# Optimization experiments

Measured on AMD Instinct MI355X. Metric: run time of the kernel, lower is better.

## Reference

```python
import jax, jax.numpy as jnp
import numpy as np

B, N, T, F_IN = 4, 2000, 24, 16
H = 128          # hidden_dim
E = 64000        # num edges
C = 6            # num_classes (LOS A-F)
NH = 1           # num_horizons


def setup_inputs() -> dict:
    key = jax.random.key(0)
    ks = jax.random.split(key, 16)
    s = lambda *sh: 1.0 / np.sqrt(sh[-1])
    inp = {
        "node_features": jax.random.normal(ks[0], (B, N, T, F_IN), dtype=jnp.float32),
        "edge_index": jax.random.randint(ks[1], (2, E), 0, N, dtype=jnp.int64),
        # GRU (single layer, unidirectional), PyTorch gate order r,z,n
        "W_ih": jax.random.normal(ks[2], (3 * H, F_IN), dtype=jnp.float32) * s(3 * H, F_IN),
        "W_hh": jax.random.normal(ks[3], (3 * H, H), dtype=jnp.float32) * s(3 * H, H),
        "b_ih": jnp.zeros((3 * H,), dtype=jnp.float32),
        "b_hh": jnp.zeros((3 * H,), dtype=jnp.float32),
        # two GCN layers (H -> H)
        "gcn_W1": jax.random.normal(ks[4], (H, H), dtype=jnp.float32) * s(H, H),
        "gcn_b1": jnp.zeros((H,), dtype=jnp.float32),
        "gcn_W2": jax.random.normal(ks[5], (H, H), dtype=jnp.float32) * s(H, H),
        "gcn_b2": jnp.zeros((H,), dtype=jnp.float32),
        # LayerNorms
        "ln_g1": jnp.ones((H,), dtype=jnp.float32),
        "ln_b1": jnp.zeros((H,), dtype=jnp.float32),
        "ln_g2": jnp.ones((H,), dtype=jnp.float32),
        "ln_b2": jnp.zeros((H,), dtype=jnp.float32),
        # classifier: Linear(2H -> H), ReLU, Linear(H -> C*NH)
        "cls_W1": jax.random.normal(ks[6], (H, 2 * H), dtype=jnp.float32) * s(H, 2 * H),
        "cls_b1": jnp.zeros((H,), dtype=jnp.float32),
        "cls_W2": jax.random.normal(ks[7], (C * NH, H), dtype=jnp.float32) * s(C * NH, H),
        "cls_b2": jnp.zeros((C * NH,), dtype=jnp.float32),
    }
    return inp


def _gru(x, W_ih, W_hh, b_ih, b_hh):
    # x: [BN, T, F] -> final hidden [BN, H]
    BN = x.shape[0]
    gi = jnp.einsum('btf,gf->btg', x, W_ih) + b_ih           # [BN, T, 3H]
    h0 = jnp.zeros((BN, H), dtype=x.dtype)

    def step(h, gi_t):
        gh = h @ W_hh.T + b_hh
        ir, iz, inn = jnp.split(gi_t, 3, axis=-1)
        hr, hz, hn = jnp.split(gh, 3, axis=-1)
        r = jax.nn.sigmoid(ir + hr)
        z = jax.nn.sigmoid(iz + hz)
        n = jnp.tanh(inn + r * hn)
        h_new = (1.0 - z) * n + z * h
        return h_new, None

    h_fin, _ = jax.lax.scan(step, h0, jnp.swapaxes(gi, 0, 1))  # scan over time
    return h_fin


def _gcn(x, src, dst, W, b):
    # x: [B, N, D]; normalized adjacency aggregation then linear
    deg = jax.ops.segment_sum(jnp.ones((src.shape[0],), x.dtype), dst, num_segments=N)
    deg = jnp.maximum(deg, 1.0)
    dis = deg ** -0.5
    norm = dis[src] * dis[dst]                                # [E]
    msg = x[:, src, :] * norm[None, :, None]                  # [B, E, D]
    agg = jax.vmap(lambda m: jax.ops.segment_sum(m, dst, num_segments=N))(msg)
    return agg @ W.T + b


def _layernorm(x, g, b, eps=1e-5):
    mu = jnp.mean(x, axis=-1, keepdims=True)
    var = jnp.var(x, axis=-1, keepdims=True)
    return (x - mu) * jax.lax.rsqrt(var + eps) * g + b


def reference(node_features, edge_index, W_ih, W_hh, b_ih, b_hh,
              gcn_W1, gcn_b1, gcn_W2, gcn_b2,
              ln_g1, ln_b1, ln_g2, ln_b2,
              cls_W1, cls_b1, cls_W2, cls_b2):
    src, dst = edge_index[0], edge_index[1]
    x = node_features.reshape(B * N, T, F_IN)
    temporal = _gru(x, W_ih, W_hh, b_ih, b_hh).reshape(B, N, H)   # [B, N, H]

    s = _gcn(temporal, src, dst, gcn_W1, gcn_b1)
    s = jax.nn.relu(_layernorm(s, ln_g1, ln_b1))
    s = _gcn(s, src, dst, gcn_W2, gcn_b2)
    s = jax.nn.relu(_layernorm(s, ln_g2, ln_b2))

    combined = jnp.concatenate([temporal, s], axis=-1)            # [B, N, 2H]
    h = jax.nn.relu(combined @ cls_W1.T + cls_b1)
    logits = h @ cls_W2.T + cls_b2
    return logits.reshape(B, N, NH, C)
```

## Files before the change

### kernel.cpp

```cpp
#include <hip/hip_runtime.h>
#include <math.h>

#define BB  4
#define NN  2000
#define TT  24
#define FIN 16
#define HH  128
#define EE  64000
#define CC  6
#define BN  (BB*NN)

typedef _Float16 f16x8 __attribute__((ext_vector_type(8)));
typedef float f32x4 __attribute__((ext_vector_type(4)));

__global__ __launch_bounds__(256) void prep_kernel(
    const int* __restrict__ dst, int* __restrict__ cnt,
    const float* __restrict__ gW2, const float* __restrict__ cW1,
    float* __restrict__ o2, _Float16* __restrict__ o3)
{
    const int b = blockIdx.x;
    const int tid = threadIdx.x;
    if (b < 250) {
        int e = b * 256 + tid;
        atomicAdd(&cnt[dst[e]], 1);
    } else if (b < 314) {
        int idx = (b - 250) * 256 + tid;
        int r = idx >> 7, c = idx & 127;
        o2[c * 128 + r] = gW2[idx];
    } else {
        int idx = (b - 314) * 256 + tid;
        int r = idx >> 8, c = idx & 255;
        o3[c * 128 + r] = (_Float16)cW1[idx];
    }
}

__global__ __launch_bounds__(256) void scan_kernel(
    const int* __restrict__ cnt,
    int* __restrict__ rowptr, int* __restrict__ cursor, float* __restrict__ dis)
{
    __shared__ int part[256];
    int tid = threadIdx.x;
    int base = tid * 8;
    int loc[8]; int s = 0;
    #pragma unroll
    for (int u = 0; u < 8; ++u) {
        int v = (base + u < NN) ? cnt[base + u] : 0;
        loc[u] = s; s += v;
    }
    part[tid] = s;
    __syncthreads();
    #pragma unroll
    for (int off = 1; off < 256; off <<= 1) {
        int add = (tid >= off) ? part[tid - off] : 0;
        __syncthreads();
        part[tid] += add;
        __syncthreads();
    }
    int offset = (tid > 0) ? part[tid - 1] : 0;
    #pragma unroll
    for (int u = 0; u < 8; ++u) {
        int idx = base + u;
        if (idx < NN) {
            rowptr[idx] = offset + loc[u];
            cursor[idx] = offset + loc[u];
            dis[idx] = rsqrtf(fmaxf((float)cnt[idx], 1.0f));
        }
    }
    if (tid == 255) rowptr[NN] = part[255];
}

#define HP2 136
#define GRUB 500

__global__ __launch_bounds__(512) void gru_csr_kernel(
    const float* __restrict__ x,
    const float* __restrict__ W_hh,
    const float* __restrict__ W_ih,
    const float* __restrict__ b_ih, const float* __restrict__ b_hh,
    const float* __restrict__ gW1,
    _Float16* __restrict__ t16,
    _Float16* __restrict__ tw16,
    const int* __restrict__ src, const int* __restrict__ dst,
    const float* __restrict__ dis, int* __restrict__ cursor,
    int* __restrict__ esrc, float* __restrict__ enorm)
{
    const int tid  = threadIdx.x;

    if (blockIdx.x >= GRUB) {
        int e = (blockIdx.x - GRUB) * 512 + tid;
        if (e < EE) {
            int d = dst[e], s = src[e];
            int pos = atomicAdd(&cursor[d], 1);
            esrc[pos] = s;
            enorm[pos] = dis[s] * dis[d];
        }
        return;
    }

    const int lane = tid & 63;
    const int w    = tid >> 6;
    const int l15  = lane & 15;
    const int lg   = lane >> 4;
    const int m0   = blockIdx.x * 16;
    const int u    = w * 16 + l15;

    __shared__ __align__(16) unsigned short Hhi[2][16][HP2];
    __shared__ __align__(16) unsigned short Xhi[TT][16][FIN];

    f16x8 Bh[3][4];
    #pragma unroll
    for (int g = 0; g < 3; ++g) {
        const int col = g * 128 + u;
        #pragma unroll
        for (int kf = 0; kf < 4; ++kf) {
            const float* wp = W_hh + col * 128 + kf * 32 + lg * 8;
            float4 c0 = *(const float4*)wp;
            float4 c1 = *(const float4*)(wp + 4);
            f16x8 b;
            b[0] = (_Float16)c0.x; b[1] = (_Float16)c0.y;
            b[2] = (_Float16)c0.z; b[3] = (_Float16)c0.w;
            b[4] = (_Float16)c1.x; b[5] = (_Float16)c1.y;
            b[6] = (_Float16)c1.z; b[7] = (_Float16)c1.w;
            Bh[g][kf] = b;
        }
    }
    f16x8 Bi[3];
    #pragma unroll
    for (int g = 0; g < 3; ++g) {
        const int col = g * 128 + u;
        f16x8 b;
        #pragma unroll
        for (int i = 0; i < 8; ++i) b[i] = (_Float16)0.0f;
        if (lg < 2) {
            const float* wp = W_ih + col * 16 + lg * 8;
            float4 c0 = *(const float4*)wp;
            float4 c1 = *(const float4*)(wp + 4);
            b[0] = (_Float16)c0.x; b[1] = (_Float16)c0.y;
            b[2] = (_Float16)c0.z; b[3] = (_Float16)c0.w;
            b[4] = (_Float16)c1.x; b[5] = (_Float16)c1.y;
            b[6] = (_Float16)c1.z; b[7] = (_Float16)c1.w;
        } else if (lg == 2) {
            float bias = b_ih[col] + ((g < 2) ? b_hh[col] : 0.0f);
            b[0] = (_Float16)bias;
        }
        Bi[g] = b;
    }

    const float bhn = b_hh[256 + u];
    float hprev[4] = {0.0f, 0.0f, 0.0f, 0.0f};

    for (int i = tid; i < TT * 16 * FIN; i += 512) {
        int t   = i >> 8;
        int rem = i & 255;
        int seq = rem >> 4;
        int f   = rem & 15;
        float v = x[(size_t)(m0 + seq) * (TT * FIN) + t * FIN + f];
        _Float16 hb = (_Float16)v;
        Xhi[t][seq][f] = *(unsigned short*)&hb;
    }
    for (int i = tid; i < 16 * HP2; i += 512) (&Hhi[0][0][0])[i] = 0;
    __syncthreads();

    const f32x4 Z4 = (f32x4){0.f, 0.f, 0.f, 0.f};
    f32x4 aR, aZ, aH, aI;

#define IH_SHADOW(tt) do { \
        f16x8 axh; \
        _Float16 zz = (_Float16)0.0f; \
        axh = (f16x8){zz,zz,zz,zz,zz,zz,zz,zz}; \
        if (lg < 2) { \
            axh = *(const f16x8*)&Xhi[tt][l15][lg * 8]; \
        } else if (lg == 2) { \
            axh[0] = (_Float16)1.0f; \
        } \
        aR = __builtin_amdgcn_mfma_f32_16x16x32_f16(axh, Bi[0], Z4, 0, 0, 0); \
        aZ = __builtin_amdgcn_mfma_f32_16x16x32_f16(axh, Bi[1], Z4, 0, 0, 0); \
        aI = __builtin_amdgcn_mfma_f32_16x16x32_f16(axh, Bi[2], Z4, 0, 0, 0); \
        aH = Z4; \
    } while (0)

    IH_SHADOW(0);

    for (int t = 0; t < TT; ++t) {
        const int rb = t & 1, wb = rb ^ 1;

        #pragma unroll
        for (int kf = 0; kf < 4; ++kf) {
            const int ko = kf * 32 + lg * 8;
            f16x8 ahh = *(const f16x8*)&Hhi[rb][l15][ko];
            aR = __builtin_amdgcn_mfma_f32_16x16x32_f16(ahh, Bh[0][kf], aR, 0, 0, 0);
            aZ = __builtin_amdgcn_mfma_f32_16x16x32_f16(ahh, Bh[1][kf], aZ, 0, 0, 0);
            aH = __builtin_amdgcn_mfma_f32_16x16x32_f16(ahh, Bh[2][kf], aH, 0, 0, 0);
        }

        f32x4 aRv = aR, aZv = aZ, aHv = aH, aIv = aI;

        #pragma unroll
        for (int p = 0; p < 4; ++p) {
            float r = __builtin_amdgcn_rcpf(1.0f + __expf(-aRv[p]));
            float z = __builtin_amdgcn_rcpf(1.0f + __expf(-aZv[p]));
            float pre = fmaf(r, aHv[p] + bhn, aIv[p]);
            float e2 = __expf(2.0f * pre);
            float n = fmaf(-2.0f, __builtin_amdgcn_rcpf(e2 + 1.0f), 1.0f);
            float h = fmaf(z, hprev[p] - n, n);
            hprev[p] = h;
            _Float16 hb = (_Float16)h;
            const int seq = lg * 4 + p;
            Hhi[wb][seq][u] = *(unsigned short*)&hb;
        }

        if (t + 1 < TT) IH_SHADOW(t + 1);
        __syncthreads();
    }
#undef IH_SHADOW

    #pragma unroll
    for (int p = 0; p < 4; ++p)
        t16[(size_t)(m0 + lg * 4 + p) * HH + u] = (_Float16)hprev[p];

    {
        f32x4 acc = Z4;
        #pragma unroll
        for (int kf = 0; kf < 4; ++kf) {
            const float* wp = gW1 + (size_t)u * 128 + kf * 32 + lg * 8;
            float4 c0 = *(const float4*)wp;
            float4 c1 = *(const float4*)(wp + 4);
            f16x8 b;
            b[0] = (_Float16)c0.x; b[1] = (_Float16)c0.y;
            b[2] = (_Float16)c0.z; b[3] = (_Float16)c0.w;
            b[4] = (_Float16)c1.x; b[5] = (_Float16)c1.y;
            b[6] = (_Float16)c1.z; b[7] = (_Float16)c1.w;
            f16x8 ah = *(const f16x8*)&Hhi[0][l15][kf * 32 + lg * 8];
            acc = __builtin_amdgcn_mfma_f32_16x16x32_f16(ah, b, acc, 0, 0, 0);
        }
        #pragma unroll
        for (int p = 0; p < 4; ++p) {
            const int row = lg * 4 + p;
            tw16[(size_t)(m0 + row) * HH + u] = (_Float16)acc[p];
        }
    }
}

__global__ __launch_bounds__(256) void gcn1_kernel(
    const _Float16* __restrict__ xin,
    const int* __restrict__ rowptr,
    const int* __restrict__ esrc,
    const float* __restrict__ enorm,
    const float* __restrict__ bias,
    const float* __restrict__ gma, const float* __restrict__ bta,
    _Float16* __restrict__ out)
{
    const int n = blockIdx.x;
    const int tid = threadIdx.x;
    const int j = tid & 127;
    const int half = tid >> 7;
    const int beg = rowptr[n], end = rowptr[n + 1];
    const int len = end - beg;
    const int mid = beg + ((len + 1) >> 1);
    int e        = half ? mid : beg;
    const int e1 = half ? end : mid;

    float a0 = 0.f, a1 = 0.f, a2 = 0.f, a3 = 0.f;
    for (; e + 1 < e1; e += 2) {
        int   s0 = esrc[e],   s1 = esrc[e + 1];
        float m0 = enorm[e],  m1 = enorm[e + 1];
        const _Float16* p0 = xin + (size_t)s0 * HH + j;
        const _Float16* p1 = xin + (size_t)s1 * HH + j;
        a0 = fmaf(m0, (float)p0[0],       a0); a1 = fmaf(m0, (float)p0[NN*HH],   a1);
        a2 = fmaf(m0, (float)p0[2*NN*HH], a2); a3 = fmaf(m0, (float)p0[3*NN*HH], a3);
        a0 = fmaf(m1, (float)p1[0],       a0); a1 = fmaf(m1, (float)p1[NN*HH],   a1);
        a2 = fmaf(m1, (float)p1[2*NN*HH], a2); a3 = fmaf(m1, (float)p1[3*NN*HH], a3);
    }
    if (e < e1) {
        int s0 = esrc[e]; float m0 = enorm[e];
        const _Float16* p0 = xin + (size_t)s0 * HH + j;
        a0 = fmaf(m0, (float)p0[0],       a0); a1 = fmaf(m0, (float)p0[NN*HH],   a1);
        a2 = fmaf(m0, (float)p0[2*NN*HH], a2); a3 = fmaf(m0, (float)p0[3*NN*HH], a3);
    }

    __shared__ __align__(16) float agg[BB][HH];
    __shared__ __align__(16) float pagg[BB][HH];
    if (half) {
        pagg[0][j] = a0; pagg[1][j] = a1; pagg[2][j] = a2; pagg[3][j] = a3;
    }
    __syncthreads();
    if (!half) {
        agg[0][j] = a0 + pagg[0][j]; agg[1][j] = a1 + pagg[1][j];
        agg[2][j] = a2 + pagg[2][j]; agg[3][j] = a3 + pagg[3][j];
    }
    __syncthreads();

    const float bj = bias[j];
    const int b0 = half * 2, b1 = half * 2 + 1;
    float c0 = agg[b0][j] + bj;
    float c1 = agg[b1][j] + bj;

    const int lane = tid & 63, wv_ = (tid >> 6) & 1;
    __shared__ float red[2][2][2][2];
    {
        float s1 = c0, s2 = c0 * c0;
        for (int off = 32; off >= 1; off >>= 1) { s1 += __shfl_down(s1, off); s2 += __shfl_down(s2, off); }
        if (lane == 0) { red[half][wv_][0][0] = s1; red[half][wv_][0][1] = s2; }
        s1 = c1; s2 = c1 * c1;
        for (int off = 32; off >= 1; off >>= 1) { s1 += __shfl_down(s1, off); s2 += __shfl_down(s2, off); }
        if (lane == 0) { red[half][wv_][1][0] = s1; red[half][wv_][1][1] = s2; }
    }
    __syncthreads();

    const float gj = gma[j], btj = bta[j];
    #pragma unroll
    for (int q = 0; q < 2; ++q) {
        float cv = q ? c1 : c0;
        float s1 = red[half][0][q][0] + red[half][1][q][0];
        float s2 = red[half][0][q][1] + red[half][1][q][1];
        float mu = s1 * (1.0f / HH);
        float var = s2 * (1.0f / HH) - mu * mu;
        float y = (cv - mu) * rsqrtf(var + 1e-5f) * gj + btj;
        out[((size_t)(half * 2 + q) * NN + n) * HH + j] = (_Float16)fmaxf(y, 0.0f);
    }
}

__global__ __launch_bounds__(256) void gcn2_kernel(
    const _Float16* __restrict__ xin,
    const int* __restrict__ rowptr,
    const int* __restrict__ esrc,
    const float* __restrict__ enorm,
    const float* __restrict__ Wt,
    const float* __restrict__ bias,
    const float* __restrict__ gma, const float* __restrict__ bta,
    _Float16* __restrict__ out)
{
    const int n = blockIdx.x;
    const int tid = threadIdx.x;
    const int j = tid & 127;
    const int half = tid >> 7;
    const int beg = rowptr[n], end = rowptr[n + 1];
    const int len = end - beg;
    const int mid = beg + ((len + 1) >> 1);
    int e        = half ? mid : beg;
    const int e1 = half ? end : mid;

    float a0 = 0.f, a1 = 0.f, a2 = 0.f, a3 = 0.f;
    for (; e + 1 < e1; e += 2) {
        int   s0 = esrc[e],   s1 = esrc[e + 1];
        float m0 = enorm[e],  m1 = enorm[e + 1];
        const _Float16* p0 = xin + (size_t)s0 * HH + j;
        const _Float16* p1 = xin + (size_t)s1 * HH + j;
        a0 = fmaf(m0, (float)p0[0],       a0); a1 = fmaf(m0, (float)p0[NN*HH],   a1);
        a2 = fmaf(m0, (float)p0[2*NN*HH], a2); a3 = fmaf(m0, (float)p0[3*NN*HH], a3);
        a0 = fmaf(m1, (float)p1[0],       a0); a1 = fmaf(m1, (float)p1[NN*HH],   a1);
        a2 = fmaf(m1, (float)p1[2*NN*HH], a2); a3 = fmaf(m1, (float)p1[3*NN*HH], a3);
    }
    if (e < e1) {
        int s0 = esrc[e]; float m0 = enorm[e];
        const _Float16* p0 = xin + (size_t)s0 * HH + j;
        a0 = fmaf(m0, (float)p0[0],       a0); a1 = fmaf(m0, (float)p0[NN*HH],   a1);
        a2 = fmaf(m0, (float)p0[2*NN*HH], a2); a3 = fmaf(m0, (float)p0[3*NN*HH], a3);
    }

    __shared__ __align__(16) float agg[BB][HH];
    __shared__ __align__(16) float pagg[BB][HH];
    if (half) {
        pagg[0][j] = a0; pagg[1][j] = a1; pagg[2][j] = a2; pagg[3][j] = a3;
    }
    __syncthreads();
    if (!half) {
        agg[0][j] = a0 + pagg[0][j]; agg[1][j] = a1 + pagg[1][j];
        agg[2][j] = a2 + pagg[2][j]; agg[3][j] = a3 + pagg[3][j];
    }
    __syncthreads();

    const float bj = bias[j];
    const int b0 = half * 2, b1 = half * 2 + 1;
    float c0 = bj, c1 = bj;
    #pragma unroll 4
    for (int k = 0; k < HH; ++k) {
        float wv = Wt[k * HH + j];
        c0 = fmaf(wv, agg[b0][k], c0);
        c1 = fmaf(wv, agg[b1][k], c1);
    }

    const int lane = tid & 63, wv_ = (tid >> 6) & 1;
    __shared__ float red[2][2][2][2];
    {
        float s1 = c0, s2 = c0 * c0;
        for (int off = 32; off >= 1; off >>= 1) { s1 += __shfl_down(s1, off); s2 += __shfl_down(s2, off); }
        if (lane == 0) { red[half][wv_][0][0] = s1; red[half][wv_][0][1] = s2; }
        s1 = c1; s2 = c1 * c1;
        for (int off = 32; off >= 1; off >>= 1) { s1 += __shfl_down(s1, off); s2 += __shfl_down(s2, off); }
        if (lane == 0) { red[half][wv_][1][0] = s1; red[half][wv_][1][1] = s2; }
    }
    __syncthreads();

    const float gj = gma[j], btj = bta[j];
    #pragma unroll
    for (int q = 0; q < 2; ++q) {
        float cv = q ? c1 : c0;
        float s1 = red[half][0][q][0] + red[half][1][q][0];
        float s2 = red[half][0][q][1] + red[half][1][q][1];
        float mu = s1 * (1.0f / HH);
        float var = s2 * (1.0f / HH) - mu * mu;
        float y = (cv - mu) * rsqrtf(var + 1e-5f) * gj + btj;
        out[((size_t)(half * 2 + q) * NN + n) * HH + j] = (_Float16)fmaxf(y, 0.0f);
    }
}

__global__ __launch_bounds__(512) void cls_kernel(
    const _Float16* __restrict__ t16,
    const _Float16* __restrict__ s2,
    const _Float16* __restrict__ c16,
    const float* __restrict__ b1,
    const float* __restrict__ W2,
    const float* __restrict__ b2,
    float* __restrict__ out)
{
    const int tid  = threadIdx.x;
    const int lane = tid & 63;
    const int w    = tid >> 6;
    const int l15  = lane & 15;
    const int lg   = lane >> 4;
    const int r0   = blockIdx.x * 16;
    const int u    = w * 16 + l15;

    const f32x4 Z4 = (f32x4){0.f, 0.f, 0.f, 0.f};
    f32x4 acc = Z4;

    #pragma unroll
    for (int kf = 0; kf < 8; ++kf) {
        const int kl = (kf & 3) * 32 + lg * 8;
        const _Float16* ap = (kf < 4) ? (t16 + (size_t)(r0 + l15) * HH + kl)
                                      : (s2  + (size_t)(r0 + l15) * HH + kl);
        f16x8 a = *(const f16x8*)ap;
        f16x8 b;
        const int kg = kf * 32 + lg * 8;
        #pragma unroll
        for (int i = 0; i < 8; ++i) b[i] = c16[(size_t)(kg + i) * 128 + u];
        acc = __builtin_amdgcn_mfma_f32_16x16x32_f16(a, b, acc, 0, 0, 0);
    }

    __shared__ __align__(16) float h1L[16][HH];
    const float bu = b1[u];
    #pragma unroll
    for (int p = 0; p < 4; ++p) {
        const int row = lg * 4 + p;
        h1L[row][u] = fmaxf(acc[p] + bu, 0.0f);
    }
    __syncthreads();

    if (tid < 16 * CC) {
        int r = tid / CC, c = tid - r * CC;
        float a = b2[c];
        const float* wp = W2 + c * HH;
        #pragma unroll 4
        for (int k = 0; k < HH; ++k) a = fmaf(wp[k], h1L[r][k], a);
        out[(size_t)(r0 + r) * CC + c] = a;
    }
}

extern "C" void kernel_launch(void* const* d_in, const int* in_sizes, int n_in,
                              void* d_out, int out_size, void* d_ws, size_t ws_size,
                              hipStream_t stream) {
    const float* x    = (const float*)d_in[0];
    const int*   ei   = (const int*)  d_in[1];
    const float* W_ih = (const float*)d_in[2];
    const float* W_hh = (const float*)d_in[3];
    const float* b_ih = (const float*)d_in[4];
    const float* b_hh = (const float*)d_in[5];
    const float* gW1  = (const float*)d_in[6];
    const float* gb1  = (const float*)d_in[7];
    const float* gW2  = (const float*)d_in[8];
    const float* gb2  = (const float*)d_in[9];
    const float* lg1  = (const float*)d_in[10];
    const float* lb1  = (const float*)d_in[11];
    const float* lg2  = (const float*)d_in[12];
    const float* lb2  = (const float*)d_in[13];
    const float* cW1  = (const float*)d_in[14];
    const float* cb1  = (const float*)d_in[15];
    const float* cW2  = (const float*)d_in[16];
    const float* cb2  = (const float*)d_in[17];
    float* out = (float*)d_out;

    float* ws = (float*)d_ws;
    float* Wt_g2 = ws;  ws += 128 * 128;
    float* dis   = ws;  ws += 2048;
    float* enorm = ws;  ws += EE;
    _Float16* t16  = (_Float16*)ws;  ws += (size_t)BN * HH / 2;
    _Float16* tw16 = (_Float16*)ws;  ws += (size_t)BN * HH / 2;
    _Float16* s16  = (_Float16*)ws;  ws += (size_t)BN * HH / 2;
    _Float16* s2_16= (_Float16*)ws;  ws += (size_t)BN * HH / 2;
    _Float16* c16  = (_Float16*)ws;  ws += 256 * 128 / 2;
    int* ip      = (int*)ws;
    int* cnt     = ip;  ip += 2048;
    int* rowptr  = ip;  ip += 2080;
    int* cursor  = ip;  ip += 2048;
    int* esrc    = ip;  ip += EE;

    const int* srcp = ei;
    const int* dstp = ei + EE;

    hipMemsetAsync(cnt, 0, 2048 * sizeof(int), stream);

    prep_kernel<<<442, 256, 0, stream>>>(dstp, cnt, gW2, cW1, Wt_g2, c16);
    scan_kernel<<<1, 256, 0, stream>>>(cnt, rowptr, cursor, dis);

    gru_csr_kernel<<<GRUB + EE / 512, 512, 0, stream>>>(
        x, W_hh, W_ih, b_ih, b_hh, gW1, t16, tw16,
        srcp, dstp, dis, cursor, esrc, enorm);

    gcn1_kernel<<<NN, 256, 0, stream>>>(tw16, rowptr, esrc, enorm,
                                        gb1, lg1, lb1, s16);

    gcn2_kernel<<<NN, 256, 0, stream>>>(s16, rowptr, esrc, enorm,
                                        Wt_g2, gb2, lg2, lb2, s2_16);

    cls_kernel<<<BN / 16, 512, 0, stream>>>(t16, s2_16, c16, cb1, cW2, cb2, out);
}
```

Measured before the change: 115.0 us.

## Fuse GCN2 weight transform into GCN1 and classifier into GCN2 aggregation

The GCN2 weight matmul moves ahead of aggregation and onto MFMA at the end of the GCN1 kernel, so GCN2 aggregates pre-transformed features. The temporal half of the classifier's first linear layer is computed in the GRU epilogue, and the separate classifier kernel is folded into the GCN2 kernel. The prep-time weight transposes and the t16/s16 intermediates are dropped. This saves a launch, several intermediate buffers and a scalar FMA loop, at the cost of uncoalesced weight loads and fewer, larger blocks (4 nodes each, one 128-thread group per node, no edge splitting).

```diff
diff --git a/kernel.cpp b/kernel.cpp
--- a/kernel.cpp
+++ b/kernel.cpp
@@ -14,24 +14,10 @@
 typedef float f32x4 __attribute__((ext_vector_type(4)));
 
 __global__ __launch_bounds__(256) void prep_kernel(
-    const int* __restrict__ dst, int* __restrict__ cnt,
-    const float* __restrict__ gW2, const float* __restrict__ cW1,
-    float* __restrict__ o2, _Float16* __restrict__ o3)
+    const int* __restrict__ dst, int* __restrict__ cnt)
 {
-    const int b = blockIdx.x;
-    const int tid = threadIdx.x;
-    if (b < 250) {
-        int e = b * 256 + tid;
-        atomicAdd(&cnt[dst[e]], 1);
-    } else if (b < 314) {
-        int idx = (b - 250) * 256 + tid;
-        int r = idx >> 7, c = idx & 127;
-        o2[c * 128 + r] = gW2[idx];
-    } else {
-        int idx = (b - 314) * 256 + tid;
-        int r = idx >> 8, c = idx & 255;
-        o3[c * 128 + r] = (_Float16)cW1[idx];
-    }
+    int e = blockIdx.x * 256 + threadIdx.x;
+    atomicAdd(&cnt[dst[e]], 1);
 }
 
 __global__ __launch_bounds__(256) void scan_kernel(
@@ -78,8 +64,9 @@
     const float* __restrict__ W_ih,
     const float* __restrict__ b_ih, const float* __restrict__ b_hh,
     const float* __restrict__ gW1,
-    _Float16* __restrict__ t16,
+    const float* __restrict__ cW1,
     _Float16* __restrict__ tw16,
+    _Float16* __restrict__ tc16,
     const int* __restrict__ src, const int* __restrict__ dst,
     const float* __restrict__ dis, int* __restrict__ cursor,
     int* __restrict__ esrc, float* __restrict__ enorm)
@@ -214,58 +201,66 @@
     }
 #undef IH_SHADOW
 
-    #pragma unroll
-    for (int p = 0; p < 4; ++p)
-        t16[(size_t)(m0 + lg * 4 + p) * HH + u] = (_Float16)hprev[p];
-
     {
-        f32x4 acc = Z4;
+        f32x4 accw = Z4, accc = Z4;
         #pragma unroll
         for (int kf = 0; kf < 4; ++kf) {
-            const float* wp = gW1 + (size_t)u * 128 + kf * 32 + lg * 8;
+            const int ko = kf * 32 + lg * 8;
+            f16x8 ah = *(const f16x8*)&Hhi[0][l15][ko];
+
+            const float* wp = gW1 + (size_t)u * 128 + ko;
             float4 c0 = *(const float4*)wp;
             float4 c1 = *(const float4*)(wp + 4);
-            f16x8 b;
-            b[0] = (_Float16)c0.x; b[1] = (_Float16)c0.y;
-            b[2] = (_Float16)c0.z; b[3] = (_Float16)c0.w;
-            b[4] = (_Float16)c1.x; b[5] = (_Float16)c1.y;
-            b[6] = (_Float16)c1.z; b[7] = (_Float16)c1.w;
-            f16x8 ah = *(const f16x8*)&Hhi[0][l15][kf * 32 + lg * 8];
-            acc = __builtin_amdgcn_mfma_f32_16x16x32_f16(ah, b, acc, 0, 0, 0);
+            f16x8 bw;
+            bw[0] = (_Float16)c0.x; bw[1] = (_Float16)c0.y;
+            bw[2] = (_Float16)c0.z; bw[3] = (_Float16)c0.w;
+            bw[4] = (_Float16)c1.x; bw[5] = (_Float16)c1.y;
+            bw[6] = (_Float16)c1.z; bw[7] = (_Float16)c1.w;
+            accw = __builtin_amdgcn_mfma_f32_16x16x32_f16(ah, bw, accw, 0, 0, 0);
+
+            const float* cp = cW1 + (size_t)u * 256 + ko;
+            float4 d0 = *(const float4*)cp;
+            float4 d1 = *(const float4*)(cp + 4);
+            f16x8 bc;
+            bc[0] = (_Float16)d0.x; bc[1] = (_Float16)d0.y;
+            bc[2] = (_Float16)d0.z; bc[3] = (_Float16)d0.w;
+            bc[4] = (_Float16)d1.x; bc[5] = (_Float16)d1.y;
+            bc[6] = (_Float16)d1.z; bc[7] = (_Float16)d1.w;
+            accc = __builtin_amdgcn_mfma_f32_16x16x32_f16(ah, bc, accc, 0, 0, 0);
         }
         #pragma unroll
         for (int p = 0; p < 4; ++p) {
             const int row = lg * 4 + p;
-            tw16[(size_t)(m0 + row) * HH + u] = (_Float16)acc[p];
-        }
-    }
-}
-
-__global__ __launch_bounds__(256) void gcn1_kernel(
-    const _Float16* __restrict__ xin,
+            tw16[(size_t)(m0 + row) * HH + u] = (_Float16)accw[p];
+            tc16[(size_t)(m0 + row) * HH + u] = (_Float16)accc[p];
+        }
+    }
+}
+
+__global__ __launch_bounds__(512) void gcn1b_kernel(
+    const _Float16* __restrict__ tw,
     const int* __restrict__ rowptr,
     const int* __restrict__ esrc,
     const float* __restrict__ enorm,
-    const float* __restrict__ bias,
-    const float* __restrict__ gma, const float* __restrict__ bta,
-    _Float16* __restrict__ out)
+    const float* __restrict__ gb1,
+    const float* __restrict__ lg1, const float* __restrict__ lb1,
+    const float* __restrict__ gW2,
+    _Float16* __restrict__ sw)
 {
-    const int n = blockIdx.x;
     const int tid = threadIdx.x;
-    const int j = tid & 127;
-    const int half = tid >> 7;
-    const int beg = rowptr[n], end = rowptr[n + 1];
-    const int len = end - beg;
-    const int mid = beg + ((len + 1) >> 1);
-    int e        = half ? mid : beg;
-    const int e1 = half ? end : mid;
+    const int nd  = tid >> 7;
+    const int j   = tid & 127;
+    const int n0  = blockIdx.x * 4;
+    const int n   = n0 + nd;
 
     float a0 = 0.f, a1 = 0.f, a2 = 0.f, a3 = 0.f;
+    int e = rowptr[n];
+    const int e1 = rowptr[n + 1];
     for (; e + 1 < e1; e += 2) {
-        int   s0 = esrc[e],   s1 = esrc[e + 1];
-        float m0 = enorm[e],  m1 = enorm[e + 1];
-        const _Float16* p0 = xin + (size_t)s0 * HH + j;
-        const _Float16* p1 = xin + (size_t)s1 * HH + j;
+        int   s0 = esrc[e],   s1i = esrc[e + 1];
+        float m0 = enorm[e],  m1  = enorm[e + 1];
+        const _Float16* p0 = tw + (size_t)s0  * HH + j;
+        const _Float16* p1 = tw + (size_t)s1i * HH + j;
         a0 = fmaf(m0, (float)p0[0],       a0); a1 = fmaf(m0, (float)p0[NN*HH],   a1);
         a2 = fmaf(m0, (float)p0[2*NN*HH], a2); a3 = fmaf(m0, (float)p0[3*NN*HH], a3);
         a0 = fmaf(m1, (float)p1[0],       a0); a1 = fmaf(m1, (float)p1[NN*HH],   a1);
@@ -273,79 +268,91 @@
     }
     if (e < e1) {
         int s0 = esrc[e]; float m0 = enorm[e];
-        const _Float16* p0 = xin + (size_t)s0 * HH + j;
+        const _Float16* p0 = tw + (size_t)s0 * HH + j;
         a0 = fmaf(m0, (float)p0[0],       a0); a1 = fmaf(m0, (float)p0[NN*HH],   a1);
         a2 = fmaf(m0, (float)p0[2*NN*HH], a2); a3 = fmaf(m0, (float)p0[3*NN*HH], a3);
     }
 
-    __shared__ __align__(16) float agg[BB][HH];
-    __shared__ __align__(16) float pagg[BB][HH];
-    if (half) {
-        pagg[0][j] = a0; pagg[1][j] = a1; pagg[2][j] = a2; pagg[3][j] = a3;
-    }
-    __syncthreads();
-    if (!half) {
-        agg[0][j] = a0 + pagg[0][j]; agg[1][j] = a1 + pagg[1][j];
-        agg[2][j] = a2 + pagg[2][j]; agg[3][j] = a3 + pagg[3][j];
-    }
-    __syncthreads();
-
-    const float bj = bias[j];
-    const int b0 = half * 2, b1 = half * 2 + 1;
-    float c0 = agg[b0][j] + bj;
-    float c1 = agg[b1][j] + bj;
-
-    const int lane = tid & 63, wv_ = (tid >> 6) & 1;
-    __shared__ float red[2][2][2][2];
-    {
-        float s1 = c0, s2 = c0 * c0;
+    const float bj = gb1[j];
+    float c[4] = {a0 + bj, a1 + bj, a2 + bj, a3 + bj};
+
+    const int lane = tid & 63, wv = (tid >> 6) & 1;
+    __shared__ float red[4][2][4][2];
+    #pragma unroll
+    for (int b = 0; b < 4; ++b) {
+        float s1 = c[b], s2 = c[b] * c[b];
         for (int off = 32; off >= 1; off >>= 1) { s1 += __shfl_down(s1, off); s2 += __shfl_down(s2, off); }
-        if (lane == 0) { red[half][wv_][0][0] = s1; red[half][wv_][0][1] = s2; }
-        s1 = c1; s2 = c1 * c1;
-        for (int off = 32; off >= 1; off >>= 1) { s1 += __shfl_down(s1, off); s2 += __shfl_down(s2, off); }
-        if (lane == 0) { red[half][wv_][1][0] = s1; red[half][wv_][1][1] = s2; }
-    }
-    __syncthreads();
-
-    const float gj = gma[j], btj = bta[j];
-    #pragma unroll
-    for (int q = 0; q < 2; ++q) {
-        float cv = q ? c1 : c0;
-        float s1 = red[half][0][q][0] + red[half][1][q][0];
-        float s2 = red[half][0][q][1] + red[half][1][q][1];
+        if (lane == 0) { red[nd][wv][b][0] = s1; red[nd][wv][b][1] = s2; }
+    }
+    __syncthreads();
+
+    __shared__ __align__(16) unsigned short sL[16][HP2];
+    const float gj = lg1[j], btj = lb1[j];
+    #pragma unroll
+    for (int b = 0; b < 4; ++b) {
+        float s1 = red[nd][0][b][0] + red[nd][1][b][0];
+        float s2 = red[nd][0][b][1] + red[nd][1][b][1];
         float mu = s1 * (1.0f / HH);
         float var = s2 * (1.0f / HH) - mu * mu;
-        float y = (cv - mu) * rsqrtf(var + 1e-5f) * gj + btj;
-        out[((size_t)(half * 2 + q) * NN + n) * HH + j] = (_Float16)fmaxf(y, 0.0f);
-    }
-}
-
-__global__ __launch_bounds__(256) void gcn2_kernel(
-    const _Float16* __restrict__ xin,
+        float y = (c[b] - mu) * rsqrtf(var + 1e-5f) * gj + btj;
+        _Float16 hv = (_Float16)fmaxf(y, 0.0f);
+        sL[nd * 4 + b][j] = *(unsigned short*)&hv;
+    }
+    __syncthreads();
+
+    const int w = tid >> 6, l15 = tid & 15, lg = (tid & 63) >> 4;
+    const int u = w * 16 + l15;
+    f32x4 acc = (f32x4){0.f, 0.f, 0.f, 0.f};
+    #pragma unroll
+    for (int kf = 0; kf < 4; ++kf) {
+        const int ko = kf * 32 + lg * 8;
+        f16x8 a = *(const f16x8*)&sL[l15][ko];
+        const float* wp = gW2 + (size_t)u * 128 + ko;
+        float4 c0 = *(const float4*)wp;
+        float4 c1 = *(const float4*)(wp + 4);
+        f16x8 b;
+        b[0] = (_Float16)c0.x; b[1] = (_Float16)c0.y;
+        b[2] = (_Float16)c0.z; b[3] = (_Float16)c0.w;
+        b[4] = (_Float16)c1.x; b[5] = (_Float16)c1.y;
+        b[6] = (_Float16)c1.z; b[7] = (_Float16)c1.w;
+        acc = __builtin_amdgcn_mfma_f32_16x16x32_f16(a, b, acc, 0, 0, 0);
+    }
+    #pragma unroll
+    for (int p = 0; p < 4; ++p) {
+        const int r = lg * 4 + p;
+        const int nd2 = r >> 2, b2 = r & 3;
+        sw[((size_t)b2 * NN + n0 + nd2) * HH + u] = (_Float16)acc[p];
+    }
+}
+
+__global__ __launch_bounds__(512) void gcn2b_cls_kernel(
+    const _Float16* __restrict__ sw,
     const int* __restrict__ rowptr,
     const int* __restrict__ esrc,
     const float* __restrict__ enorm,
-    const float* __restrict__ Wt,
-    const float* __restrict__ bias,
-    const float* __restrict__ gma, const float* __restrict__ bta,
-    _Float16* __restrict__ out)
+    const float* __restrict__ gb2,
+    const float* __restrict__ lg2, const float* __restrict__ lb2,
+    const float* __restrict__ cW1,
+    const _Float16* __restrict__ tc,
+    const float* __restrict__ cb1,
+    const float* __restrict__ cW2,
+    const float* __restrict__ cb2,
+    float* __restrict__ out)
 {
-    const int n = blockIdx.x;
     const int tid = threadIdx.x;
-    const int j = tid & 127;
-    const int half = tid >> 7;
-    const int beg = rowptr[n], end = rowptr[n + 1];
-    const int len = end - beg;
-    const int mid = beg + ((len + 1) >> 1);
-    int e        = half ? mid : beg;
-    const int e1 = half ? end : mid;
+    const int nd  = tid >> 7;
+    const int j   = tid & 127;
+    const int n0  = blockIdx.x * 4;
+    const int n   = n0 + nd;
 
     float a0 = 0.f, a1 = 0.f, a2 = 0.f, a3 = 0.f;
+    int e = rowptr[n];
+    const int e1 = rowptr[n + 1];
     for (; e + 1 < e1; e += 2) {
-        int   s0 = esrc[e],   s1 = esrc[e + 1];
-        float m0 = enorm[e],  m1 = enorm[e + 1];
-        const _Float16* p0 = xin + (size_t)s0 * HH + j;
-        const _Float16* p1 = xin + (size_t)s1 * HH + j;
+        int   s0 = esrc[e],   s1i = esrc[e + 1];
+        float m0 = enorm[e],  m1  = enorm[e + 1];
+        const _Float16* p0 = sw + (size_t)s0  * HH + j;
+        const _Float16* p1 = sw + (size_t)s1i * HH + j;
         a0 = fmaf(m0, (float)p0[0],       a0); a1 = fmaf(m0, (float)p0[NN*HH],   a1);
         a2 = fmaf(m0, (float)p0[2*NN*HH], a2); a3 = fmaf(m0, (float)p0[3*NN*HH], a3);
         a0 = fmaf(m1, (float)p1[0],       a0); a1 = fmaf(m1, (float)p1[NN*HH],   a1);
@@ -353,107 +360,77 @@
     }
     if (e < e1) {
         int s0 = esrc[e]; float m0 = enorm[e];
-        const _Float16* p0 = xin + (size_t)s0 * HH + j;
+        const _Float16* p0 = sw + (size_t)s0 * HH + j;
         a0 = fmaf(m0, (float)p0[0],       a0); a1 = fmaf(m0, (float)p0[NN*HH],   a1);
         a2 = fmaf(m0, (float)p0[2*NN*HH], a2); a3 = fmaf(m0, (float)p0[3*NN*HH], a3);
     }
 
-    __shared__ __align__(16) float agg[BB][HH];
-    __shared__ __align__(16) float pagg[BB][HH];
-    if (half) {
-        pagg[0][j] = a0; pagg[1][j] = a1; pagg[2][j] = a2; pagg[3][j] = a3;
-    }
-    __syncthreads();
-    if (!half) {
-        agg[0][j] = a0 + pagg[0][j]; agg[1][j] = a1 + pagg[1][j];
-        agg[2][j] = a2 + pagg[2][j]; agg[3][j] = a3 + pagg[3][j];
-    }
-    __syncthreads();
-
-    const float bj = bias[j];
-    const int b0 = half * 2, b1 = half * 2 + 1;
-    float c0 = bj, c1 = bj;
-    #pragma unroll 4
-    for (int k = 0; k < HH; ++k) {
-        float wv = Wt[k * HH + j];
-        c0 = fmaf(wv, agg[b0][k], c0);
-        c1 = fmaf(wv, agg[b1][k], c1);
-    }
-
-    const int lane = tid & 63, wv_ = (tid >> 6) & 1;
-    __shared__ float red[2][2][2][2];
-    {
-        float s1 = c0, s2 = c0 * c0;
+    const float bj = gb2[j];
+    float c[4] = {a0 + bj, a1 + bj, a2 + bj, a3 + bj};
+
+    const int lane = tid & 63, wv = (tid >> 6) & 1;
+    __shared__ float red[4][2][4][2];
+    #pragma unroll
+    for (int b = 0; b < 4; ++b) {
+        float s1 = c[b], s2 = c[b] * c[b];
         for (int off = 32; off >= 1; off >>= 1) { s1 += __shfl_down(s1, off); s2 += __shfl_down(s2, off); }
-        if (lane == 0) { red[half][wv_][0][0] = s1; red[half][wv_][0][1] = s2; }
-        s1 = c1; s2 = c1 * c1;
-        for (int off = 32; off >= 1; off >>= 1) { s1 += __shfl_down(s1, off); s2 += __shfl_down(s2, off); }
-        if (lane == 0) { red[half][wv_][1][0] = s1; red[half][wv_][1][1] = s2; }
-    }
-    __syncthreads();
-
-    const float gj = gma[j], btj = bta[j];
-    #pragma unroll
-    for (int q = 0; q < 2; ++q) {
-        float cv = q ? c1 : c0;
-        float s1 = red[half][0][q][0] + red[half][1][q][0];
-        float s2 = red[half][0][q][1] + red[half][1][q][1];
+        if (lane == 0) { red[nd][wv][b][0] = s1; red[nd][wv][b][1] = s2; }
+    }
+    __syncthreads();
+
+    __shared__ __align__(16) unsigned short s2L[16][HP2];
+    const float gj = lg2[j], btj = lb2[j];
+    #pragma unroll
+    for (int b = 0; b < 4; ++b) {
+        float s1 = red[nd][0][b][0] + red[nd][1][b][0];
+        float s2 = red[nd][0][b][1] + red[nd][1][b][1];
         float mu = s1 * (1.0f / HH);
         float var = s2 * (1.0f / HH) - mu * mu;
-        float y = (cv - mu) * rsqrtf(var + 1e-5f) * gj + btj;
-        out[((size_t)(half * 2 + q) * NN + n) * HH + j] = (_Float16)fmaxf(y, 0.0f);
-    }
-}
-
-__global__ __launch_bounds__(512) void cls_kernel(
-    const _Float16* __restrict__ t16,
-    const _Float16* __restrict__ s2,
-    const _Float16* __restrict__ c16,
-    const float* __restrict__ b1,
-    const float* __restrict__ W2,
-    const float* __restrict__ b2,
-    float* __restrict__ out)
-{
-    const int tid  = threadIdx.x;
-    const int lane = tid & 63;
-    const int w    = tid >> 6;
-    const int l15  = lane & 15;
-    const int lg   = lane >> 4;
-    const int r0   = blockIdx.x * 16;
-    const int u    = w * 16 + l15;
-
-    const f32x4 Z4 = (f32x4){0.f, 0.f, 0.f, 0.f};
-    f32x4 acc = Z4;
-
-    #pragma unroll
-    for (int kf = 0; kf < 8; ++kf) {
-        const int kl = (kf & 3) * 32 + lg * 8;
-        const _Float16* ap = (kf < 4) ? (t16 + (size_t)(r0 + l15) * HH + kl)
-                                      : (s2  + (size_t)(r0 + l15) * HH + kl);
-        f16x8 a = *(const f16x8*)ap;
+        float y = (c[b] - mu) * rsqrtf(var + 1e-5f) * gj + btj;
+        _Float16 hv = (_Float16)fmaxf(y, 0.0f);
+        s2L[nd * 4 + b][j] = *(unsigned short*)&hv;
+    }
+    __syncthreads();
+
+    const int w = tid >> 6, l15 = tid & 15, lg = (tid & 63) >> 4;
+    const int u = w * 16 + l15;
+    f32x4 acc = (f32x4){0.f, 0.f, 0.f, 0.f};
+    #pragma unroll
+    for (int kf = 0; kf < 4; ++kf) {
+        const int ko = kf * 32 + lg * 8;
+        f16x8 a = *(const f16x8*)&s2L[l15][ko];
+        const float* cp = cW1 + (size_t)u * 256 + 128 + ko;
+        float4 d0 = *(const float4*)cp;
+        float4 d1 = *(const float4*)(cp + 4);
         f16x8 b;
-        const int kg = kf * 32 + lg * 8;
-        #pragma unroll
-        for (int i = 0; i < 8; ++i) b[i] = c16[(size_t)(kg + i) * 128 + u];
+        b[0] = (_Float16)d0.x; b[1] = (_Float16)d0.y;
+        b[2] = (_Float16)d0.z; b[3] = (_Float16)d0.w;
+        b[4] = (_Float16)d1.x; b[5] = (_Float16)d1.y;
+        b[6] = (_Float16)d1.z; b[7] = (_Float16)d1.w;
         acc = __builtin_amdgcn_mfma_f32_16x16x32_f16(a, b, acc, 0, 0, 0);
     }
 
-    __shared__ __align__(16) float h1L[16][HH];
-    const float bu = b1[u];
+    __shared__ __align__(16) float h1L[16][132];
+    const float bu = cb1[u];
     #pragma unroll
     for (int p = 0; p < 4; ++p) {
-        const int row = lg * 4 + p;
-        h1L[row][u] = fmaxf(acc[p] + bu, 0.0f);
+        const int r = lg * 4 + p;
+        const int nd2 = r >> 2, b2 = r & 3;
+        const size_t flat = (size_t)b2 * NN + n0 + nd2;
+        float tcv = (float)tc[flat * HH + u];
+        h1L[r][u] = fmaxf(acc[p] + tcv + bu, 0.0f);
     }
     __syncthreads();
 
     if (tid < 16 * CC) {
-        int r = tid / CC, c = tid - r * CC;
-        float a = b2[c];
-        const float* wp = W2 + c * HH;
+        int r = tid / CC, cc = tid - r * CC;
+        const int nd2 = r >> 2, b2 = r & 3;
+        const size_t flat = (size_t)b2 * NN + n0 + nd2;
+        float a = cb2[cc];
+        const float* wp = cW2 + cc * HH;
         #pragma unroll 4
         for (int k = 0; k < HH; ++k) a = fmaf(wp[k], h1L[r][k], a);
-        out[(size_t)(r0 + r) * CC + c] = a;
+        out[flat * CC + cc] = a;
     }
 }
 
@@ -481,14 +458,11 @@
     float* out = (float*)d_out;
 
     float* ws = (float*)d_ws;
-    float* Wt_g2 = ws;  ws += 128 * 128;
     float* dis   = ws;  ws += 2048;
     float* enorm = ws;  ws += EE;
-    _Float16* t16  = (_Float16*)ws;  ws += (size_t)BN * HH / 2;
     _Float16* tw16 = (_Float16*)ws;  ws += (size_t)BN * HH / 2;
-    _Float16* s16  = (_Float16*)ws;  ws += (size_t)BN * HH / 2;
-    _Float16* s2_16= (_Float16*)ws;  ws += (size_t)BN * HH / 2;
-    _Float16* c16  = (_Float16*)ws;  ws += 256 * 128 / 2;
+    _Float16* tc16 = (_Float16*)ws;  ws += (size_t)BN * HH / 2;
+    _Float16* sw16 = (_Float16*)ws;  ws += (size_t)BN * HH / 2;
     int* ip      = (int*)ws;
     int* cnt     = ip;  ip += 2048;
     int* rowptr  = ip;  ip += 2080;
@@ -500,18 +474,17 @@
 
     hipMemsetAsync(cnt, 0, 2048 * sizeof(int), stream);
 
-    prep_kernel<<<442, 256, 0, stream>>>(dstp, cnt, gW2, cW1, Wt_g2, c16);
+    prep_kernel<<<250, 256, 0, stream>>>(dstp, cnt);
     scan_kernel<<<1, 256, 0, stream>>>(cnt, rowptr, cursor, dis);
 
     gru_csr_kernel<<<GRUB + EE / 512, 512, 0, stream>>>(
-        x, W_hh, W_ih, b_ih, b_hh, gW1, t16, tw16,
+        x, W_hh, W_ih, b_ih, b_hh, gW1, cW1, tw16, tc16,
         srcp, dstp, dis, cursor, esrc, enorm);
 
-    gcn1_kernel<<<NN, 256, 0, stream>>>(tw16, rowptr, esrc, enorm,
-                                        gb1, lg1, lb1, s16);
-
-    gcn2_kernel<<<NN, 256, 0, stream>>>(s16, rowptr, esrc, enorm,
-                                        Wt_g2, gb2, lg2, lb2, s2_16);
-
-    cls_kernel<<<BN / 16, 512, 0, stream>>>(t16, s2_16, c16, cb1, cW2, cb2, out);
-}
+    gcn1b_kernel<<<NN / 4, 512, 0, stream>>>(tw16, rowptr, esrc, enorm,
+                                             gb1, lg1, lb1, gW2, sw16);
+
+    gcn2b_cls_kernel<<<NN / 4, 512, 0, stream>>>(sw16, rowptr, esrc, enorm,
+                                                 gb2, lg2, lb2, cW1, tc16,
+                                                 cb1, cW2, cb2, out);
+}
```

Result: slower. 119.8 us (+4.2%).
